# Kernel tuning notes

Hardware: AMD Instinct MI355X
Metric: run time of the kernel (lower is better)

## Reference

```python
import jax, jax.numpy as jnp
import numpy as np
from jax import lax

H = 32  # hidden_dim

def _lstm_layer(x_tbd, W_ih, W_hh, b_ih, b_hh):
    """x_tbd: [T, B, D]. Returns all hidden states [T, B, H]. PyTorch gate order i,f,g,o."""
    T, B, _ = x_tbd.shape
    # Precompute input contribution for all timesteps (one big GEMM)
    xW = jnp.einsum('tbd,gd->tbg', x_tbd, W_ih) + (b_ih + b_hh)  # [T, B, 4H]
    W_hh_T = W_hh.T  # [H, 4H]

    def step(carry, xw):
        h, c = carry
        gates = xw + h @ W_hh_T  # [B, 4H]
        i, f, g, o = jnp.split(gates, 4, axis=-1)
        i = jax.nn.sigmoid(i)
        f = jax.nn.sigmoid(f)
        g = jnp.tanh(g)
        o = jax.nn.sigmoid(o)
        c = f * c + i * g
        h = o * jnp.tanh(c)
        return (h, c), h

    h0 = jnp.zeros((B, H), x_tbd.dtype)
    (_, _), hs = lax.scan(step, (h0, h0), xW)
    return hs  # [T, B, H]


def setup_inputs() -> dict:
    key = jax.random.key(0)
    ks = jax.random.split(key, 12)
    s = 0.1  # keep gates out of saturation
    return {
        'x': jax.random.normal(ks[0], (4096, 512, 4), jnp.float32),
        'W_ih0': jax.random.normal(ks[1], (4 * H, 4), jnp.float32) * s,
        'W_hh0': jax.random.normal(ks[2], (4 * H, H), jnp.float32) * s,
        'b_ih0': jax.random.normal(ks[3], (4 * H,), jnp.float32) * s,
        'b_hh0': jax.random.normal(ks[4], (4 * H,), jnp.float32) * s,
        'W_ih1': jax.random.normal(ks[5], (4 * H, H), jnp.float32) * s,
        'W_hh1': jax.random.normal(ks[6], (4 * H, H), jnp.float32) * s,
        'b_ih1': jax.random.normal(ks[7], (4 * H,), jnp.float32) * s,
        'b_hh1': jax.random.normal(ks[8], (4 * H,), jnp.float32) * s,
        'W_out': jax.random.normal(ks[9], (1, H), jnp.float32) * s,
        'b_out': jax.random.normal(ks[10], (1,), jnp.float32) * s,
    }


def reference(x, W_ih0, W_hh0, b_ih0, b_hh0, W_ih1, W_hh1, b_ih1, b_hh1, W_out, b_out):
    # x: [B, T, D] (batch_first). Eval mode -> inter-layer dropout is identity.
    x_tbd = jnp.transpose(x, (1, 0, 2))  # [T, B, D]
    h1 = _lstm_layer(x_tbd, W_ih0, W_hh0, b_ih0, b_hh0)  # [T, B, H]
    h2 = _lstm_layer(h1, W_ih1, W_hh1, b_ih1, b_hh1)     # [T, B, H]
    last = h2[-1]  # [B, H] == out[:, -1, :]
    return last @ W_out.T + b_out  # [B, 1]
```

## Files before the change

### kernel.cpp

```cpp
#include <hip/hip_runtime.h>
#include <cmath>

constexpr int T   = 512;
constexpr int D   = 4;
constexpr int H   = 32;
constexpr int BT  = 16;
constexpr int BLK = 256;

constexpr float LOG2E     = 1.44269504088896340736f;
constexpr float NEG2LOG2E = -2.88539008177792681472f;

typedef short bf8 __attribute__((ext_vector_type(8)));
typedef short s4v __attribute__((ext_vector_type(4)));
typedef float f4  __attribute__((ext_vector_type(4)));

static __device__ __forceinline__ short bf16_rtn(float v) {
    unsigned u = __float_as_uint(v);
    u += 0x7FFFu + ((u >> 16) & 1u);
    return (short)(u >> 16);
}
static __device__ __forceinline__ float sigm2(float a) {
    return __builtin_amdgcn_rcpf(1.0f + __builtin_amdgcn_exp2f(a));
}

__global__ __launch_bounds__(BLK, 1) void lstm_bf16(
    const float* __restrict__ x,
    const float* __restrict__ W_ih0, const float* __restrict__ W_hh0,
    const float* __restrict__ b_ih0, const float* __restrict__ b_hh0,
    const float* __restrict__ W_ih1, const float* __restrict__ W_hh1,
    const float* __restrict__ b_ih1, const float* __restrict__ b_hh1,
    const float* __restrict__ W_out, const float* __restrict__ b_out,
    float* __restrict__ out)
{
    __shared__ __align__(16) short h0b[2][16][56];
    __shared__ __align__(16) short h1b[2][16][56];
    __shared__ __align__(16) float h1f[16][36];

    const int tid   = threadIdx.x;
    const int w     = tid >> 6;
    const int lane  = tid & 63;
    const int q     = lane >> 4;
    const int nl    = lane & 15;
    const int layer = w >> 1;
    const int ug    = (w & 1) << 4;
    const int b0    = blockIdx.x * BT;

    for (int idx = tid; idx < 2 * 16 * 56; idx += BLK) {
        (&h0b[0][0][0])[idx] = 0;
        (&h1b[0][0][0])[idx] = 0;
    }

    const float* W1 = layer ? W_ih1 : W_hh0;
    bf8 w1[4], w2[4];
    f4  bias[4];
    #pragma unroll
    for (int g = 0; g < 4; ++g) {
        const float sc = (g == 2) ? NEG2LOG2E : -LOG2E;
        const int row = 32 * g + ug + nl;
        #pragma unroll
        for (int j = 0; j < 8; ++j) {
            w1[g][j] = bf16_rtn(W1[row * H + 8 * q + j] * sc);
            float v2 = layer ? W_hh1[row * H + 8 * q + j]
                             : ((q == 0 && j < 4) ? W_ih0[row * D + j] : 0.0f);
            w2[g][j] = bf16_rtn(v2 * sc);
        }
        #pragma unroll
        for (int r = 0; r < 4; ++r) {
            const int gr = 32 * g + ug + 4 * q + r;
            bias[g][r] = sc * (layer ? (b_ih1[gr] + b_hh1[gr])
                                     : (b_ih0[gr] + b_hh0[gr]));
        }
    }

    const float4* xp = (const float4*)(x + (size_t)(b0 + nl) * (T * D));
    float4 xcur;
    if (layer == 0) xcur = xp[0];

    float c[4] = {0.0f, 0.0f, 0.0f, 0.0f};

    __syncthreads();

    #pragma unroll 1
    for (int i = 0; i <= T; ++i) {
        const int rb = i & 1, wb = rb ^ 1;

        bf8 b2;
        if (layer == 0) {
            bf8 z = {0,0,0,0,0,0,0,0};
            b2 = z;
            b2[0] = bf16_rtn(xcur.x);
            b2[1] = bf16_rtn(xcur.y);
            b2[2] = bf16_rtn(xcur.z);
            b2[3] = bf16_rtn(xcur.w);
            xcur = xp[(i + 1 < T) ? (i + 1) : (T - 1)];
        } else {
            b2 = *(const bf8*)&h1b[rb][nl][8 * q];
        }
        bf8 b1 = *(const bf8*)&h0b[rb][nl][8 * q];

        f4 acc[4];
        #pragma unroll
        for (int g = 0; g < 4; ++g) {
            f4 A = __builtin_amdgcn_mfma_f32_16x16x32_bf16(w2[g], b2, bias[g], 0, 0, 0);
            A    = __builtin_amdgcn_mfma_f32_16x16x32_bf16(w1[g], b1, A,       0, 0, 0);
            acc[g] = A;
        }

        const bool act = layer ? (i >= 1) : (i < T);
        if (act) {
            s4v hh;
            float hv[4];
            #pragma unroll
            for (int r = 0; r < 4; ++r) {
                float iv = sigm2(acc[0][r]);
                float fv = sigm2(acc[1][r]);
                float gv = fmaf(sigm2(acc[2][r]), 2.0f, -1.0f);
                float ov = sigm2(acc[3][r]);
                c[r] = fmaf(fv, c[r], iv * gv);
                float th = fmaf(sigm2(c[r] * NEG2LOG2E), 2.0f, -1.0f);
                hv[r] = ov * th;
                hh[r] = bf16_rtn(hv[r]);
            }
            if (layer == 0) {
                *(s4v*)&h0b[wb][nl][ug + 4 * q] = hh;
            } else {
                *(s4v*)&h1b[wb][nl][ug + 4 * q] = hh;
                if (i == T) {
                    float4 hw; hw.x = hv[0]; hw.y = hv[1]; hw.z = hv[2]; hw.w = hv[3];
                    *(float4*)&h1f[nl][ug + 4 * q] = hw;
                }
            }
        }
        __syncthreads();
    }

    if (tid < BT) {
        float acc = b_out[0];
        #pragma unroll
        for (int u = 0; u < H; ++u) acc = fmaf(W_out[u], h1f[tid][u], acc);
        out[b0 + tid] = acc;
    }
}

extern "C" void kernel_launch(void* const* d_in, const int* in_sizes, int n_in,
                              void* d_out, int out_size, void* d_ws, size_t ws_size,
                              hipStream_t stream) {
    const float* x     = (const float*)d_in[0];
    const float* W_ih0 = (const float*)d_in[1];
    const float* W_hh0 = (const float*)d_in[2];
    const float* b_ih0 = (const float*)d_in[3];
    const float* b_hh0 = (const float*)d_in[4];
    const float* W_ih1 = (const float*)d_in[5];
    const float* W_hh1 = (const float*)d_in[6];
    const float* b_ih1 = (const float*)d_in[7];
    const float* b_hh1 = (const float*)d_in[8];
    const float* W_out = (const float*)d_in[9];
    const float* b_out = (const float*)d_in[10];
    float* out = (float*)d_out;

    const int B = out_size;
    lstm_bf16<<<B / BT, BLK, 0, stream>>>(x, W_ih0, W_hh0, b_ih0, b_hh0,
                                          W_ih1, W_hh1, b_ih1, b_hh1,
                                          W_out, b_out, out);
}
```

Baseline: 334.7 us.

## Duplicate MFMA across wave pairs and split gate activations; fuse sigmoid reciprocals

Doubles the block to 8 waves so each (layer, unit-group) is handled by two waves. Both waves redundantly compute the same MFMAs, but each applies the gate nonlinearities to only two of the four accumulator rows, shortening the serial per-step activation chain. The activation math is also rewritten to share reciprocals: i*g and o*tanh(c) each use one rcp of a product of denominators, cutting transcendental ops. The cost is doubled MFMA and register work, more waves taking part in each per-step barrier, and slightly different rounding.

Result: slower. 365.1 us (+9.1%).

```diff
diff --git a/kernel.cpp b/kernel.cpp
--- a/kernel.cpp
+++ b/kernel.cpp
@@ -5,25 +5,23 @@
 constexpr int D   = 4;
 constexpr int H   = 32;
 constexpr int BT  = 16;
-constexpr int BLK = 256;
+constexpr int BLK = 512;
 
 constexpr float LOG2E     = 1.44269504088896340736f;
 constexpr float NEG2LOG2E = -2.88539008177792681472f;
 
 typedef short bf8 __attribute__((ext_vector_type(8)));
-typedef short s4v __attribute__((ext_vector_type(4)));
+typedef short s2v __attribute__((ext_vector_type(2)));
 typedef float f4  __attribute__((ext_vector_type(4)));
+typedef float f2  __attribute__((ext_vector_type(2)));
 
 static __device__ __forceinline__ short bf16_rtn(float v) {
     unsigned u = __float_as_uint(v);
     u += 0x7FFFu + ((u >> 16) & 1u);
     return (short)(u >> 16);
 }
-static __device__ __forceinline__ float sigm2(float a) {
-    return __builtin_amdgcn_rcpf(1.0f + __builtin_amdgcn_exp2f(a));
-}
 
-__global__ __launch_bounds__(BLK, 1) void lstm_bf16(
+__global__ __launch_bounds__(BLK, 1) void lstm_bf16d(
     const float* __restrict__ x,
     const float* __restrict__ W_ih0, const float* __restrict__ W_hh0,
     const float* __restrict__ b_ih0, const float* __restrict__ b_hh0,
@@ -41,8 +39,9 @@
     const int lane  = tid & 63;
     const int q     = lane >> 4;
     const int nl    = lane & 15;
-    const int layer = w >> 1;
-    const int ug    = (w & 1) << 4;
+    const int layer = w >> 2;
+    const int ug    = ((w >> 1) & 1) << 4;
+    const int sub   = w & 1;
     const int b0    = blockIdx.x * BT;
 
     for (int idx = tid; idx < 2 * 16 * 56; idx += BLK) {
@@ -76,7 +75,7 @@
     float4 xcur;
     if (layer == 0) xcur = xp[0];
 
-    float c[4] = {0.0f, 0.0f, 0.0f, 0.0f};
+    float c[2] = {0.0f, 0.0f};
 
     __syncthreads();
 
@@ -108,26 +107,31 @@
 
         const bool act = layer ? (i >= 1) : (i < T);
         if (act) {
-            s4v hh;
-            float hv[4];
+            s2v hh;
+            float hv[2];
             #pragma unroll
-            for (int r = 0; r < 4; ++r) {
-                float iv = sigm2(acc[0][r]);
-                float fv = sigm2(acc[1][r]);
-                float gv = fmaf(sigm2(acc[2][r]), 2.0f, -1.0f);
-                float ov = sigm2(acc[3][r]);
-                c[r] = fmaf(fv, c[r], iv * gv);
-                float th = fmaf(sigm2(c[r] * NEG2LOG2E), 2.0f, -1.0f);
-                hv[r] = ov * th;
+            for (int r = 0; r < 2; ++r) {
+                const int rr = 2 * sub + r;
+                float ei = __builtin_amdgcn_exp2f(acc[0][rr]);
+                float ef = __builtin_amdgcn_exp2f(acc[1][rr]);
+                float eg = __builtin_amdgcn_exp2f(acc[2][rr]);
+                float eo = __builtin_amdgcn_exp2f(acc[3][rr]);
+                float rig = __builtin_amdgcn_rcpf((1.0f + ei) * (1.0f + eg));
+                float rf  = __builtin_amdgcn_rcpf(1.0f + ef);
+                c[r] = fmaf(c[r], rf, (1.0f - eg) * rig);
+                float ec = __builtin_amdgcn_exp2f(c[r] * NEG2LOG2E);
+                float rot = __builtin_amdgcn_rcpf((1.0f + eo) * (1.0f + ec));
+                hv[r] = (1.0f - ec) * rot;
                 hh[r] = bf16_rtn(hv[r]);
             }
+            const int uo = ug + 4 * q + 2 * sub;
             if (layer == 0) {
-                *(s4v*)&h0b[wb][nl][ug + 4 * q] = hh;
+                *(s2v*)&h0b[wb][nl][uo] = hh;
             } else {
-                *(s4v*)&h1b[wb][nl][ug + 4 * q] = hh;
+                *(s2v*)&h1b[wb][nl][uo] = hh;
                 if (i == T) {
-                    float4 hw; hw.x = hv[0]; hw.y = hv[1]; hw.z = hv[2]; hw.w = hv[3];
-                    *(float4*)&h1f[nl][ug + 4 * q] = hw;
+                    f2 hw; hw.x = hv[0]; hw.y = hv[1];
+                    *(f2*)&h1f[nl][uo] = hw;
                 }
             }
         }
@@ -159,7 +163,7 @@
     float* out = (float*)d_out;
 
     const int B = out_size;
-    lstm_bf16<<<B / BT, BLK, 0, stream>>>(x, W_ih0, W_hh0, b_ih0, b_hh0,
-                                          W_ih1, W_hh1, b_ih1, b_hh1,
-                                          W_out, b_out, out);
+    lstm_bf16d<<<B / BT, BLK, 0, stream>>>(x, W_ih0, W_hh0, b_ih0, b_hh0,
+                                           W_ih1, W_hh1, b_ih1, b_hh1,
+                                           W_out, b_out, out);
 }
```

## Stage bf16 inputs in LDS, merge gate reciprocals, unroll time loop by two

Applied to the files above, without the earlier changes.

Preloads each block's whole input sequence into shared memory as bf16, so the recurrent loop does an LDS read instead of a global load plus conversion every step. It rewrites the gate math so sigmoid and tanh combinations share two reciprocals per element instead of five. It also unrolls the time loop by two so the double-buffer indices become constants. In exchange it uses about 64KB of LDS, pays a prologue load, and the merged denominators may lose a little precision or overflow for large exponents.

Result: faster. 295.5 us (-11.7%).

```diff
diff --git a/kernel.cpp b/kernel.cpp
--- a/kernel.cpp
+++ b/kernel.cpp
@@ -10,6 +10,8 @@
 constexpr float LOG2E     = 1.44269504088896340736f;
 constexpr float NEG2LOG2E = -2.88539008177792681472f;
 
+constexpr int XSTRIDE = 2052;
+
 typedef short bf8 __attribute__((ext_vector_type(8)));
 typedef short s4v __attribute__((ext_vector_type(4)));
 typedef float f4  __attribute__((ext_vector_type(4)));
@@ -19,11 +21,8 @@
     u += 0x7FFFu + ((u >> 16) & 1u);
     return (short)(u >> 16);
 }
-static __device__ __forceinline__ float sigm2(float a) {
-    return __builtin_amdgcn_rcpf(1.0f + __builtin_amdgcn_exp2f(a));
-}
 
-__global__ __launch_bounds__(BLK, 1) void lstm_bf16(
+__global__ __launch_bounds__(BLK, 1) void lstm_bf16s(
     const float* __restrict__ x,
     const float* __restrict__ W_ih0, const float* __restrict__ W_hh0,
     const float* __restrict__ b_ih0, const float* __restrict__ b_hh0,
@@ -32,6 +31,7 @@
     const float* __restrict__ W_out, const float* __restrict__ b_out,
     float* __restrict__ out)
 {
+    __shared__ __align__(16) short xbf[16 * XSTRIDE];
     __shared__ __align__(16) short h0b[2][16][56];
     __shared__ __align__(16) short h1b[2][16][56];
     __shared__ __align__(16) float h1f[16][36];
@@ -45,6 +45,15 @@
     const int ug    = (w & 1) << 4;
     const int b0    = blockIdx.x * BT;
 
+    for (int idx = tid; idx < 16 * T; idx += BLK) {
+        const int col = idx >> 9;
+        const int t   = idx & (T - 1);
+        float4 xv = *(const float4*)(x + ((size_t)(b0 + col) * T + t) * D);
+        s4v v;
+        v[0] = bf16_rtn(xv.x); v[1] = bf16_rtn(xv.y);
+        v[2] = bf16_rtn(xv.z); v[3] = bf16_rtn(xv.w);
+        *(s4v*)&xbf[col * XSTRIDE + t * 4] = v;
+    }
     for (int idx = tid; idx < 2 * 16 * 56; idx += BLK) {
         (&h0b[0][0][0])[idx] = 0;
         (&h1b[0][0][0])[idx] = 0;
@@ -72,27 +81,18 @@
         }
     }
 
-    const float4* xp = (const float4*)(x + (size_t)(b0 + nl) * (T * D));
-    float4 xcur;
-    if (layer == 0) xcur = xp[0];
-
     float c[4] = {0.0f, 0.0f, 0.0f, 0.0f};
 
     __syncthreads();
 
-    #pragma unroll 1
-    for (int i = 0; i <= T; ++i) {
-        const int rb = i & 1, wb = rb ^ 1;
-
+    auto body = [&](const int i, const int rb, const int wb) {
         bf8 b2;
         if (layer == 0) {
+            const int t = (i < T) ? i : (T - 1);
+            s4v xv = *(const s4v*)&xbf[nl * XSTRIDE + t * 4];
             bf8 z = {0,0,0,0,0,0,0,0};
             b2 = z;
-            b2[0] = bf16_rtn(xcur.x);
-            b2[1] = bf16_rtn(xcur.y);
-            b2[2] = bf16_rtn(xcur.z);
-            b2[3] = bf16_rtn(xcur.w);
-            xcur = xp[(i + 1 < T) ? (i + 1) : (T - 1)];
+            b2[0] = xv[0]; b2[1] = xv[1]; b2[2] = xv[2]; b2[3] = xv[3];
         } else {
             b2 = *(const bf8*)&h1b[rb][nl][8 * q];
         }
@@ -112,13 +112,17 @@
             float hv[4];
             #pragma unroll
             for (int r = 0; r < 4; ++r) {
-                float iv = sigm2(acc[0][r]);
-                float fv = sigm2(acc[1][r]);
-                float gv = fmaf(sigm2(acc[2][r]), 2.0f, -1.0f);
-                float ov = sigm2(acc[3][r]);
-                c[r] = fmaf(fv, c[r], iv * gv);
-                float th = fmaf(sigm2(c[r] * NEG2LOG2E), 2.0f, -1.0f);
-                hv[r] = ov * th;
+                float ei = __builtin_amdgcn_exp2f(acc[0][r]);
+                float ef = __builtin_amdgcn_exp2f(acc[1][r]);
+                float eg = __builtin_amdgcn_exp2f(acc[2][r]);
+                float eo = __builtin_amdgcn_exp2f(acc[3][r]);
+                float D1 = 1.0f + ef;
+                float D2 = (1.0f + ei) * (1.0f + eg);
+                float rD = __builtin_amdgcn_rcpf(D1 * D2);
+                c[r] = (fmaf(c[r], D2, (1.0f - eg) * D1)) * rD;
+                float ec = __builtin_amdgcn_exp2f(c[r] * NEG2LOG2E);
+                float ro = __builtin_amdgcn_rcpf((1.0f + eo) * (1.0f + ec));
+                hv[r] = (1.0f - ec) * ro;
                 hh[r] = bf16_rtn(hv[r]);
             }
             if (layer == 0) {
@@ -132,7 +136,14 @@
             }
         }
         __syncthreads();
+    };
+
+    #pragma unroll 1
+    for (int i = 0; i < T; i += 2) {
+        body(i,     0, 1);
+        body(i + 1, 1, 0);
     }
+    body(T, 0, 1);
 
     if (tid < BT) {
         float acc = b_out[0];
@@ -159,7 +170,7 @@
     float* out = (float*)d_out;
 
     const int B = out_size;
-    lstm_bf16<<<B / BT, BLK, 0, stream>>>(x, W_ih0, W_hh0, b_ih0, b_hh0,
-                                          W_ih1, W_hh1, b_ih1, b_hh1,
-                                          W_out, b_out, out);
+    lstm_bf16s<<<B / BT, BLK, 0, stream>>>(x, W_ih0, W_hh0, b_ih0, b_hh0,
+                                           W_ih1, W_hh1, b_ih1, b_hh1,
+                                           W_out, b_out, out);
 }
```
